# Performance work log

Hardware: AMD Instinct MI355X
Metric: run time of the kernel (lower is better)

## Reference

```python
import jax, jax.numpy as jnp
import numpy as np

HIDDEN = 256
NUM_REGIMES = 4

def setup_inputs() -> dict:
    key = jax.random.key(0)
    ks = jax.random.split(key, 9)
    B, D, A = 65536, 256, 128
    x = jax.random.normal(ks[0], (B, D), dtype=jnp.float32)
    regime = jax.random.randint(ks[1], (B,), 0, NUM_REGIMES).astype(jnp.float32)
    x = x.at[:, -1].set(regime)  # last feature holds the discrete regime id
    s1 = 1.0 / np.sqrt(D)
    s2 = 1.0 / np.sqrt(HIDDEN)
    W1 = jax.random.uniform(ks[2], (D, HIDDEN), jnp.float32, -s1, s1)
    b1 = jax.random.uniform(ks[3], (HIDDEN,), jnp.float32, -s1, s1)
    W2 = jax.random.uniform(ks[4], (HIDDEN, HIDDEN), jnp.float32, -s2, s2)
    b2 = jax.random.uniform(ks[5], (HIDDEN,), jnp.float32, -s2, s2)
    Wh = jax.random.uniform(ks[6], (NUM_REGIMES, HIDDEN, A), jnp.float32, -s2, s2)
    bh = jax.random.uniform(ks[7], (NUM_REGIMES, A), jnp.float32, -s2, s2)
    log_std = jnp.zeros((A,), dtype=jnp.float32)
    return {"x": x, "W1": W1, "b1": b1, "W2": W2, "b2": b2,
            "Wh": Wh, "bh": bh, "log_std": log_std}

def reference(x, W1, b1, W2, b2, Wh, bh, log_std):
    # regime index from last feature column (hard routing)
    regime_idx = x[:, -1].astype(jnp.int32)  # [B]
    # backbone MLP: Linear-ReLU-Linear-ReLU
    h = jax.nn.relu(x @ W1 + b1)
    feats = jax.nn.relu(h @ W2 + b2)  # [B, HIDDEN]
    # compute all 4 regime heads densely, then gather per-sample head output
    raw_all = jnp.einsum('bh,rha->bra', feats, Wh) + bh[None, :, :]  # [B, 4, A]
    raw = jnp.take_along_axis(raw_all, regime_idx[:, None, None], axis=1)[:, 0, :]  # [B, A]
    mean = raw * 0.1
    std = jnp.clip(jnp.exp(log_std), 1e-3, 1.0)
    std = jnp.broadcast_to(std[None, :], mean.shape)
    return mean, std
```

## Files before the change

### kernel.cpp

```cpp
#include <hip/hip_runtime.h>
#include <hip/hip_bf16.h>
#include <cstddef>


typedef unsigned short u16;
typedef unsigned int   u32;

using bf16x8 = __attribute__((ext_vector_type(8))) __bf16;
using f32x4  = __attribute__((ext_vector_type(4))) float;

#define BM      32
#define LDSW    264
#define THREADS 512

__device__ __forceinline__ u16 f2bf(float f) {
  return __builtin_bit_cast(u16, (__bf16)f);
}

__global__ void prep_weights(const float* __restrict__ W1,
                             const float* __restrict__ W2,
                             const float* __restrict__ Wh,
                             u16* __restrict__ ws) {
  int i = blockIdx.x * 256 + threadIdx.x;
  {
    int j  = i & 7, l = (i >> 3) & 63, kk = (i >> 9) & 7;
    int nb = (i >> 12) & 1, w = i >> 13;
    int n = w * 32 + nb * 16 + (l & 15);
    int k = kk * 32 + ((l >> 4) << 3) + j;
    ws[i]         = f2bf(W1[k * 256 + n]);
    ws[65536 + i] = f2bf(W2[k * 256 + n]);
  }
#pragma unroll
  for (int t = 0; t < 2; ++t) {
    int idx = i + t * 65536;
    int j  = idx & 7, l = (idx >> 3) & 63, kk = (idx >> 9) & 7;
    int nb = (idx >> 12) & 3, w = idx >> 14;
    int c = w * 64 + nb * 16 + (l & 15);
    int k = kk * 32 + ((l >> 4) << 3) + j;
    int r = c >> 7, a = c & 127;
    ws[131072 + idx] = f2bf(Wh[(r * 256 + k) * 128 + a]);
  }
}

__device__ __forceinline__ void gemm32(f32x4 acc[2][2], const u16* A,
                                       const u16* __restrict__ Wp,
                                       int ar, int kg, int lane) {
#pragma unroll
  for (int kk = 0; kk < 8; ++kk) {
    const int k = kk * 32 + kg;
    bf16x8 a[2], b[2];
#pragma unroll
    for (int m = 0; m < 2; ++m)
      a[m] = *(const bf16x8*)&A[(m * 16 + ar) * LDSW + k];
#pragma unroll
    for (int nb = 0; nb < 2; ++nb)
      b[nb] = *(const bf16x8*)&Wp[((nb * 8 + kk) * 64 + lane) * 8];
#pragma unroll
    for (int m = 0; m < 2; ++m)
#pragma unroll
      for (int nb = 0; nb < 2; ++nb)
        acc[m][nb] = __builtin_amdgcn_mfma_f32_16x16x32_bf16(a[m], b[nb], acc[m][nb], 0, 0, 0);
  }
}

__device__ __forceinline__ void epilogue_relu(f32x4 acc[2][2], const float* __restrict__ bias,
                                              u16* O, int n0, int ar, int orow) {
#pragma unroll
  for (int nb = 0; nb < 2; ++nb) {
    const int col = n0 + nb * 16 + ar;
    const float bv = bias[col];
#pragma unroll
    for (int m = 0; m < 2; ++m) {
#pragma unroll
      for (int j = 0; j < 4; ++j) {
        float v = acc[m][nb][j] + bv;
        v = v > 0.f ? v : 0.f;
        O[(m * 16 + orow + j) * LDSW + col] = f2bf(v);
      }
    }
  }
}

__global__ __launch_bounds__(THREADS, 4) void actor_main(
    const float* __restrict__ x,
    const float* __restrict__ b1, const float* __restrict__ b2,
    const float* __restrict__ bh, const float* __restrict__ log_std,
    const u16* __restrict__ wbf,
    float* __restrict__ out_mean, float* __restrict__ out_std) {
  __shared__ u16 bufA[BM * LDSW];
  __shared__ u16 bufB[BM * LDSW];
  __shared__ int s_regime[BM];

  const int tid  = threadIdx.x;
  const int lane = tid & 63;
  const int wave = tid >> 6;
  const int row0 = blockIdx.x * BM;
  const int ar   = lane & 15;
  const int kg   = (lane >> 4) * 8;
  const int orow = (lane >> 4) * 4;
  const int n0   = wave * 32;

  {
    const float4* xg = (const float4*)(x + (size_t)row0 * 256);
#pragma unroll
    for (int it = 0; it < 4; ++it) {
      const int i = tid + it * THREADS;
      float4 v = xg[i];
      int row = i >> 6, c4 = (i & 63) << 2;
      ushort4 b;
      b.x = f2bf(v.x); b.y = f2bf(v.y); b.z = f2bf(v.z); b.w = f2bf(v.w);
      *(ushort4*)&bufA[row * LDSW + c4] = b;
      if (c4 == 252) s_regime[row] = (int)v.w;
    }
  }

  {
    const int c4 = (tid & 31) << 2;
    float4 s;
    s.x = fminf(fmaxf(expf(log_std[c4 + 0]), 1e-3f), 1.0f);
    s.y = fminf(fmaxf(expf(log_std[c4 + 1]), 1e-3f), 1.0f);
    s.z = fminf(fmaxf(expf(log_std[c4 + 2]), 1e-3f), 1.0f);
    s.w = fminf(fmaxf(expf(log_std[c4 + 3]), 1e-3f), 1.0f);
#pragma unroll
    for (int i = tid; i < BM * 32; i += THREADS) {
      int row = i >> 5;
      *(float4*)&out_std[(size_t)(row0 + row) * 128 + c4] = s;
    }
  }
  __syncthreads();

  {
    f32x4 acc[2][2] = {};
    gemm32(acc, bufA, wbf + wave * 8192, ar, kg, lane);
    epilogue_relu(acc, b1, bufB, n0, ar, orow);
  }
  __syncthreads();

  {
    f32x4 acc[2][2] = {};
    gemm32(acc, bufB, wbf + 65536 + wave * 8192, ar, kg, lane);
    epilogue_relu(acc, b2, bufA, n0, ar, orow);
  }
  __syncthreads();

  {
    const u16* __restrict__ Wp3 = wbf + 131072 + wave * 16384;
    f32x4 acc[2][4] = {};
#pragma unroll
    for (int kk = 0; kk < 8; ++kk) {
      const int k = kk * 32 + kg;
      bf16x8 a[2], b[4];
#pragma unroll
      for (int nb = 0; nb < 4; ++nb)
        b[nb] = *(const bf16x8*)&Wp3[((nb * 8 + kk) * 64 + lane) * 8];
#pragma unroll
      for (int m = 0; m < 2; ++m)
        a[m] = *(const bf16x8*)&bufA[(m * 16 + ar) * LDSW + k];
#pragma unroll
      for (int m = 0; m < 2; ++m)
#pragma unroll
        for (int nb = 0; nb < 4; ++nb)
          acc[m][nb] = __builtin_amdgcn_mfma_f32_16x16x32_bf16(a[m], b[nb], acc[m][nb], 0, 0, 0);
    }
    const int head = wave >> 1;
    const int c0   = (wave & 1) * 64;
#pragma unroll
    for (int nb = 0; nb < 4; ++nb) {
      const int acol = c0 + nb * 16 + ar;
      const float bhv = bh[head * 128 + acol];
#pragma unroll
      for (int m = 0; m < 2; ++m) {
#pragma unroll
        for (int j = 0; j < 4; ++j) {
          const int row = m * 16 + orow + j;
          if (s_regime[row] == head)
            out_mean[(size_t)(row0 + row) * 128 + acol] = 0.1f * (acc[m][nb][j] + bhv);
        }
      }
    }
  }
}

extern "C" void kernel_launch(void* const* d_in, const int* in_sizes, int n_in,
                              void* d_out, int out_size, void* d_ws, size_t ws_size,
                              hipStream_t stream) {
  const float* x  = (const float*)d_in[0];
  const float* W1 = (const float*)d_in[1];
  const float* b1 = (const float*)d_in[2];
  const float* W2 = (const float*)d_in[3];
  const float* b2 = (const float*)d_in[4];
  const float* Wh = (const float*)d_in[5];
  const float* bh = (const float*)d_in[6];
  const float* ls = (const float*)d_in[7];

  const int B = in_sizes[0] / 256;
  float* out_mean = (float*)d_out;
  float* out_std  = out_mean + (size_t)B * 128;
  u16* wbf = (u16*)d_ws;

  hipLaunchKernelGGL(prep_weights, dim3(256), dim3(256), 0, stream, W1, W2, Wh, wbf);
  hipLaunchKernelGGL(actor_main, dim3(B / BM), dim3(THREADS), 0, stream,
                     x, b1, b2, bh, ls, wbf, out_mean, out_std);
}
```

Baseline: 81.53 us.

## Double row tile to 64 with 1024 threads, 16 waves splitting columns

Increases the per-block row tile from 32 to 64 and the block size to 16 waves, each wave now owning 16 output columns per backbone layer (32 for the head) across all 64 rows. The weight prep layout is reshuffled to match the new per-wave column slices. Each weight fragment loaded from global memory is reused across four row sub-tiles instead of two, halving weight traffic per row. In exchange LDS per block doubles and blocks are larger, which may reduce occupancy and increase barrier cost. The x-load loop still runs 4 iterations, which with 1024 threads covers all 64 rows.

Measured after the change: 70.83 us. -13.1%, faster.

```diff
diff --git a/kernel.cpp b/kernel.cpp
--- a/kernel.cpp
+++ b/kernel.cpp
@@ -9,9 +9,9 @@
 using bf16x8 = __attribute__((ext_vector_type(8))) __bf16;
 using f32x4  = __attribute__((ext_vector_type(4))) float;
 
-#define BM      32
+#define BM      64
 #define LDSW    264
-#define THREADS 512
+#define THREADS 1024
 
 __device__ __forceinline__ u16 f2bf(float f) {
   return __builtin_bit_cast(u16, (__bf16)f);
@@ -24,8 +24,8 @@
   int i = blockIdx.x * 256 + threadIdx.x;
   {
     int j  = i & 7, l = (i >> 3) & 63, kk = (i >> 9) & 7;
-    int nb = (i >> 12) & 1, w = i >> 13;
-    int n = w * 32 + nb * 16 + (l & 15);
+    int w  = (i >> 12) & 15;
+    int n = w * 16 + (l & 15);
     int k = kk * 32 + ((l >> 4) << 3) + j;
     ws[i]         = f2bf(W1[k * 256 + n]);
     ws[65536 + i] = f2bf(W2[k * 256 + n]);
@@ -34,49 +34,41 @@
   for (int t = 0; t < 2; ++t) {
     int idx = i + t * 65536;
     int j  = idx & 7, l = (idx >> 3) & 63, kk = (idx >> 9) & 7;
-    int nb = (idx >> 12) & 3, w = idx >> 14;
-    int c = w * 64 + nb * 16 + (l & 15);
+    int nb = (idx >> 12) & 1, w = (idx >> 13) & 15;
+    int c = w * 32 + nb * 16 + (l & 15);
     int k = kk * 32 + ((l >> 4) << 3) + j;
     int r = c >> 7, a = c & 127;
     ws[131072 + idx] = f2bf(Wh[(r * 256 + k) * 128 + a]);
   }
 }
 
-__device__ __forceinline__ void gemm32(f32x4 acc[2][2], const u16* A,
+__device__ __forceinline__ void gemm16(f32x4 acc[4], const u16* A,
                                        const u16* __restrict__ Wp,
                                        int ar, int kg, int lane) {
 #pragma unroll
   for (int kk = 0; kk < 8; ++kk) {
     const int k = kk * 32 + kg;
-    bf16x8 a[2], b[2];
+    bf16x8 b = *(const bf16x8*)&Wp[(kk * 64 + lane) * 8];
+    bf16x8 a[4];
 #pragma unroll
-    for (int m = 0; m < 2; ++m)
+    for (int m = 0; m < 4; ++m)
       a[m] = *(const bf16x8*)&A[(m * 16 + ar) * LDSW + k];
 #pragma unroll
-    for (int nb = 0; nb < 2; ++nb)
-      b[nb] = *(const bf16x8*)&Wp[((nb * 8 + kk) * 64 + lane) * 8];
-#pragma unroll
-    for (int m = 0; m < 2; ++m)
-#pragma unroll
-      for (int nb = 0; nb < 2; ++nb)
-        acc[m][nb] = __builtin_amdgcn_mfma_f32_16x16x32_bf16(a[m], b[nb], acc[m][nb], 0, 0, 0);
+    for (int m = 0; m < 4; ++m)
+      acc[m] = __builtin_amdgcn_mfma_f32_16x16x32_bf16(a[m], b, acc[m], 0, 0, 0);
   }
 }
 
-__device__ __forceinline__ void epilogue_relu(f32x4 acc[2][2], const float* __restrict__ bias,
-                                              u16* O, int n0, int ar, int orow) {
+__device__ __forceinline__ void epilogue_relu(f32x4 acc[4], const float* __restrict__ bias,
+                                              u16* O, int col, int orow) {
+  const float bv = bias[col];
 #pragma unroll
-  for (int nb = 0; nb < 2; ++nb) {
-    const int col = n0 + nb * 16 + ar;
-    const float bv = bias[col];
+  for (int m = 0; m < 4; ++m) {
 #pragma unroll
-    for (int m = 0; m < 2; ++m) {
-#pragma unroll
-      for (int j = 0; j < 4; ++j) {
-        float v = acc[m][nb][j] + bv;
-        v = v > 0.f ? v : 0.f;
-        O[(m * 16 + orow + j) * LDSW + col] = f2bf(v);
-      }
+    for (int j = 0; j < 4; ++j) {
+      float v = acc[m][j] + bv;
+      v = v > 0.f ? v : 0.f;
+      O[(m * 16 + orow + j) * LDSW + col] = f2bf(v);
     }
   }
 }
@@ -98,7 +90,7 @@
   const int ar   = lane & 15;
   const int kg   = (lane >> 4) * 8;
   const int orow = (lane >> 4) * 4;
-  const int n0   = wave * 32;
+  const int n0   = wave * 16;
 
   {
     const float4* xg = (const float4*)(x + (size_t)row0 * 256);
@@ -130,46 +122,46 @@
   __syncthreads();
 
   {
-    f32x4 acc[2][2] = {};
-    gemm32(acc, bufA, wbf + wave * 8192, ar, kg, lane);
-    epilogue_relu(acc, b1, bufB, n0, ar, orow);
+    f32x4 acc[4] = {};
+    gemm16(acc, bufA, wbf + wave * 4096, ar, kg, lane);
+    epilogue_relu(acc, b1, bufB, n0 + ar, orow);
   }
   __syncthreads();
 
   {
-    f32x4 acc[2][2] = {};
-    gemm32(acc, bufB, wbf + 65536 + wave * 8192, ar, kg, lane);
-    epilogue_relu(acc, b2, bufA, n0, ar, orow);
+    f32x4 acc[4] = {};
+    gemm16(acc, bufB, wbf + 65536 + wave * 4096, ar, kg, lane);
+    epilogue_relu(acc, b2, bufA, n0 + ar, orow);
   }
   __syncthreads();
 
   {
-    const u16* __restrict__ Wp3 = wbf + 131072 + wave * 16384;
-    f32x4 acc[2][4] = {};
+    const u16* __restrict__ Wp3 = wbf + 131072 + wave * 8192;
+    f32x4 acc[4][2] = {};
 #pragma unroll
     for (int kk = 0; kk < 8; ++kk) {
       const int k = kk * 32 + kg;
-      bf16x8 a[2], b[4];
+      bf16x8 a[4], b[2];
 #pragma unroll
-      for (int nb = 0; nb < 4; ++nb)
+      for (int nb = 0; nb < 2; ++nb)
         b[nb] = *(const bf16x8*)&Wp3[((nb * 8 + kk) * 64 + lane) * 8];
 #pragma unroll
-      for (int m = 0; m < 2; ++m)
+      for (int m = 0; m < 4; ++m)
         a[m] = *(const bf16x8*)&bufA[(m * 16 + ar) * LDSW + k];
 #pragma unroll
-      for (int m = 0; m < 2; ++m)
+      for (int m = 0; m < 4; ++m)
 #pragma unroll
-        for (int nb = 0; nb < 4; ++nb)
+        for (int nb = 0; nb < 2; ++nb)
           acc[m][nb] = __builtin_amdgcn_mfma_f32_16x16x32_bf16(a[m], b[nb], acc[m][nb], 0, 0, 0);
     }
-    const int head = wave >> 1;
-    const int c0   = (wave & 1) * 64;
+    const int head = wave >> 2;
+    const int c0   = (wave & 3) * 32;
 #pragma unroll
-    for (int nb = 0; nb < 4; ++nb) {
+    for (int nb = 0; nb < 2; ++nb) {
       const int acol = c0 + nb * 16 + ar;
       const float bhv = bh[head * 128 + acol];
 #pragma unroll
-      for (int m = 0; m < 2; ++m) {
+      for (int m = 0; m < 4; ++m) {
 #pragma unroll
         for (int j = 0; j < 4; ++j) {
           const int row = m * 16 + orow + j;
```
